# Optimization experiments

Hardware: AMD Instinct MI355X
Metric: run time of the kernel (lower is better)

The kernel has to match this reference:

```python
import jax, jax.numpy as jnp
import numpy as np

B, L, EMB, U, V = 128, 64, 512, 1024, 50257
BN_EPS = 0.001


def setup_inputs() -> dict:
    key = jax.random.key(0)
    ks = jax.random.split(key, 20)
    s = 0.02
    return {
        "x": jax.random.randint(ks[0], (B, 1), 0, V, dtype=jnp.int64),
        "features": jax.random.normal(ks[1], (B, L, EMB), jnp.float32),
        "hidden": jax.random.normal(ks[2], (1, B, U), jnp.float32),
        "emb_table": jax.random.normal(ks[3], (V, EMB), jnp.float32) * s,
        "Uattn_w": jax.random.normal(ks[4], (U, EMB), jnp.float32) * s,
        "Uattn_b": jnp.zeros((U,), jnp.float32),
        "Wattn_w": jax.random.normal(ks[5], (U, U), jnp.float32) * s,
        "Wattn_b": jnp.zeros((U,), jnp.float32),
        "Vattn_w": jax.random.normal(ks[6], (1, U), jnp.float32) * s,
        "Vattn_b": jnp.zeros((1,), jnp.float32),
        "W_ih": jax.random.normal(ks[7], (3 * U, U), jnp.float32) * s,
        "W_hh": jax.random.normal(ks[8], (3 * U, U), jnp.float32) * s,
        "b_ih": jnp.zeros((3 * U,), jnp.float32),
        "b_hh": jnp.zeros((3 * U,), jnp.float32),
        "fc_w": jax.random.normal(ks[9], (U, U), jnp.float32) * s,
        "fc_b": jnp.zeros((U,), jnp.float32),
        "bn_gamma": jnp.ones((U,), jnp.float32),
        "bn_beta": jnp.zeros((U,), jnp.float32),
        "bn_mean": jnp.zeros((U,), jnp.float32),
        "bn_var": jnp.ones((U,), jnp.float32),
        "fc2_w": jax.random.normal(ks[10], (V, U), jnp.float32) * s,
        "fc2_b": jnp.zeros((V,), jnp.float32),
    }


def reference(x, features, hidden, emb_table, Uattn_w, Uattn_b, Wattn_w, Wattn_b,
              Vattn_w, Vattn_b, W_ih, W_hh, b_ih, b_hh, fc_w, fc_b,
              bn_gamma, bn_beta, bn_mean, bn_var, fc2_w, fc2_b):
    h = hidden[0]  # [B, U]
    # Bahdanau attention
    Uf = jnp.einsum('ble,ue->blu', features, Uattn_w) + Uattn_b        # [B,L,U]
    Wh = h @ Wattn_w.T + Wattn_b                                        # [B,U]
    score = jnp.tanh(Uf + Wh[:, None, :]) @ Vattn_w.T + Vattn_b        # [B,L,1]
    attn = jax.nn.softmax(score, axis=1)                                # [B,L,1]
    ctx = jnp.sum(attn * features, axis=1)                              # [B,EMB]
    # embed token and concat -> GRU input (seq len 1)
    e = emb_table[x[:, 0]]                                              # [B,EMB]
    gin = jnp.concatenate([ctx, e], axis=-1)                            # [B,U]
    # single-step GRU (PyTorch gate convention)
    gi = gin @ W_ih.T + b_ih                                            # [B,3U]
    gh = h @ W_hh.T + b_hh                                              # [B,3U]
    i_r, i_z, i_n = jnp.split(gi, 3, axis=-1)
    h_r, h_z, h_n = jnp.split(gh, 3, axis=-1)
    r = jax.nn.sigmoid(i_r + h_r)
    z = jax.nn.sigmoid(i_z + h_z)
    n = jnp.tanh(i_n + r * h_n)
    h_new = (1.0 - z) * n + z * h                                       # [B,U]
    # head: fc -> (dropout: identity in eval) -> BN (eval) -> fc2
    y = h_new @ fc_w.T + fc_b
    y = (y - bn_mean) * jax.lax.rsqrt(bn_var + BN_EPS) * bn_gamma + bn_beta
    logits = y @ fc2_w.T + fc2_b                                        # [B,V]
    return logits, h_new[None, :, :], attn
```

## Files before the change

### kernel.cpp

```cpp
#include <hip/hip_runtime.h>

typedef short bf8 __attribute__((ext_vector_type(8)));
typedef float f32x4 __attribute__((ext_vector_type(4)));

__device__ inline short f2bfs(float f) {
    unsigned u = __builtin_bit_cast(unsigned, f);
    u += 0x7FFFu + ((u >> 16) & 1u);
    return (short)(u >> 16);
}

__device__ inline unsigned pk2(float x, float y) {
    return (unsigned)(unsigned short)f2bfs(x) |
           ((unsigned)(unsigned short)f2bfs(y) << 16);
}

__device__ inline float bf2f(short s) {
    unsigned u = ((unsigned)(unsigned short)s) << 16;
    return __builtin_bit_cast(float, u);
}

__device__ inline bf8 cvt_frag(f32x4 lo, f32x4 hi) {
    union { bf8 v; unsigned u[4]; } r;
    r.u[0] = pk2(lo[0], lo[1]);
    r.u[1] = pk2(lo[2], lo[3]);
    r.u[2] = pk2(hi[0], hi[1]);
    r.u[3] = pk2(hi[2], hi[3]);
    return r.v;
}

__device__ inline float fast_tanh(float x) {
    x = fminf(fmaxf(x, -15.f), 15.f);
    float e = __expf(2.f * x);
    return (e - 1.f) / (e + 1.f);
}

__device__ inline void gl_lds16(const void* g, void* l) {
    __builtin_amdgcn_global_load_lds(
        (const __attribute__((address_space(1))) unsigned int*)g,
        (__attribute__((address_space(3))) unsigned int*)l,
        16, 0, 0);
}

#define BAR() asm volatile("s_barrier" ::: "memory")

template<int N> __device__ __forceinline__ void waitvm() {
    if constexpr (N == 8)      asm volatile("s_waitcnt vmcnt(8)"  ::: "memory");
    else if constexpr (N == 6) asm volatile("s_waitcnt vmcnt(6)"  ::: "memory");
    else if constexpr (N == 4) asm volatile("s_waitcnt vmcnt(4)"  ::: "memory");
    else if constexpr (N == 3) asm volatile("s_waitcnt vmcnt(3)"  ::: "memory");
    else                       asm volatile("s_waitcnt vmcnt(0)"  ::: "memory");
}

#define MFMA16 __builtin_amdgcn_mfma_f32_16x16x32_bf16

template<int EPI, int BM_, bool OBF>
__device__ __forceinline__ void gemm_body(
    char* smem,
    const short* __restrict__ A, const float* __restrict__ W,
    const float* __restrict__ bias, void* __restrict__ Cv,
    int N, int K, int lda, int n0, int m0,
    const float* __restrict__ q0, const float* __restrict__ q1,
    const float* __restrict__ q2, const float* __restrict__ q3,
    float* __restrict__ score)
{
    constexpr int FM  = BM_ / 32;
    constexpr int ATS = BM_ * 64;
    constexpr int LPT = (BM_ == 128) ? 4 : 3;

    const int lane = threadIdx.x & 63;
    const int wave = threadIdx.x >> 6;
    const int wm0  = (wave >> 1) * (BM_ / 2);
    const int wn0  = (wave & 1) * 32;
    const int lr   = lane & 15;
    const int g    = lane >> 4;

    f32x4 acc[FM][2] = {};

    auto stage = [&](int buf, int k0) {
        char* sA = smem + buf * ATS;
        char* sW = smem + 3 * ATS + buf * 8192;
        #pragma unroll
        for (int cc = 0; cc < BM_ / 64; ++cc) {
            int c  = wave * (BM_ / 64) + cc;
            int r  = c * 16 + (lane >> 2);
            int ss = (lane & 3) ^ ((r >> 1) & 3);
            gl_lds16(&A[(size_t)(m0 + r) * lda + k0 + ss * 8], sA + c * 1024);
        }
        #pragma unroll
        for (int cc = 0; cc < 2; ++cc) {
            int c  = wave * 2 + cc;
            int r  = c * 8 + (lane >> 3);
            int ss = (lane & 7) ^ (r & 7);
            int rg = n0 + r; rg = rg < N ? rg : N - 1;
            gl_lds16(&W[(size_t)rg * K + k0 + ss * 4], sW + c * 1024);
        }
    };

    auto compute = [&](int buf) {
        char* sA = smem + buf * ATS;
        char* sW = smem + 3 * ATS + buf * 8192;
        bf8 av[FM], bv[2];
        #pragma unroll
        for (int i = 0; i < FM; ++i) {
            int ra = wm0 + i * 16 + lr;
            int sl = g ^ ((ra >> 1) & 3);
            av[i] = *reinterpret_cast<const bf8*>(sA + ra * 64 + sl * 16);
        }
        #pragma unroll
        for (int j = 0; j < 2; ++j) {
            int rb = wn0 + j * 16 + lr;
            int l0 = (2 * g)     ^ (rb & 7);
            int l1 = (2 * g + 1) ^ (rb & 7);
            f32x4 lo = *reinterpret_cast<const f32x4*>(sW + rb * 128 + l0 * 16);
            f32x4 hi = *reinterpret_cast<const f32x4*>(sW + rb * 128 + l1 * 16);
            bv[j] = cvt_frag(lo, hi);
        }
        #pragma unroll
        for (int i = 0; i < FM; ++i)
            #pragma unroll
            for (int j = 0; j < 2; ++j)
                acc[i][j] = MFMA16(av[i], bv[j], acc[i][j], 0, 0, 0);
    };

    const int nt = K >> 5;
    stage(0, 0); stage(1, 32);
    int bs = 2, bc = 0;
    for (int t = 0; t < nt - 2; ++t) {
        stage(bs, (t + 2) << 5);
        bs = (bs == 2) ? 0 : bs + 1;
        waitvm<2 * LPT>(); BAR();
        compute(bc);
        bc = (bc == 2) ? 0 : bc + 1;
        BAR();
    }
    waitvm<1 * LPT>(); BAR(); compute(bc); bc = (bc == 2) ? 0 : bc + 1; BAR();
    waitvm<0>();       BAR(); compute(bc);

    if constexpr (EPI == 2) {
        #pragma unroll
        for (int i = 0; i < FM; ++i) {
            #pragma unroll
            for (int r = 0; r < 4; ++r) {
                int m = m0 + wm0 + i * 16 + g * 4 + r;
                int bidx = m >> 6;
                float s = 0.f;
                #pragma unroll
                for (int j = 0; j < 2; ++j) {
                    int n = n0 + wn0 + j * 16 + lr;
                    s += fast_tanh(acc[i][j][r] + bias[n] + q0[(size_t)bidx * N + n]) * q1[n];
                }
                #pragma unroll
                for (int off = 1; off < 16; off <<= 1)
                    s += __shfl_xor(s, off);
                if (lr == 0) atomicAdd(&score[m], s);
            }
        }
    } else {
        #pragma unroll
        for (int j = 0; j < 2; ++j) {
            int n = n0 + wn0 + j * 16 + lr;
            if (n >= N) continue;
            float bn_ = bias[n];
            float sc = 1.f, sh = 0.f;
            if constexpr (EPI == 1) {
                sc = q0[n] * rsqrtf(q3[n] + 1e-3f);
                sh = q1[n] - q2[n] * sc;
            }
            #pragma unroll
            for (int i = 0; i < FM; ++i) {
                #pragma unroll
                for (int r = 0; r < 4; ++r) {
                    int m = m0 + wm0 + i * 16 + g * 4 + r;
                    float v = acc[i][j][r] + bn_;
                    if constexpr (EPI == 1) v = v * sc + sh;
                    if constexpr (OBF) ((short*)Cv)[(size_t)m * N + n] = f2bfs(v);
                    else               ((float*)Cv)[(size_t)m * N + n] = v;
                }
            }
        }
    }
}

template<int EPI, int BM_, bool OBF>
__global__ __launch_bounds__(256) void gemm_k(
    const short* __restrict__ A, const float* __restrict__ W,
    const float* __restrict__ bias, void* __restrict__ Cv,
    int N, int K, int lda,
    const float* __restrict__ q0, const float* __restrict__ q1,
    const float* __restrict__ q2, const float* __restrict__ q3,
    float* __restrict__ score)
{
    __shared__ __align__(1024) char smem[3 * BM_ * 64 + 3 * 8192];
    gemm_body<EPI, BM_, OBF>(smem, A, W, bias, Cv, N, K, lda,
                             blockIdx.x * 64, blockIdx.y * BM_,
                             q0, q1, q2, q3, score);
}

__global__ __launch_bounds__(256) void gemm_dual(
    const short* __restrict__ A0, const float* __restrict__ W0,
    const float* __restrict__ b0, float* __restrict__ C0,
    const short* __restrict__ A1, const float* __restrict__ W1,
    const float* __restrict__ b1, float* __restrict__ C1,
    int N, int K, int lda)
{
    __shared__ __align__(1024) char smem[3 * 64 * 64 + 3 * 8192];
    if (blockIdx.z == 0)
        gemm_body<0, 64, false>(smem, A0, W0, b0, C0, N, K, lda,
                                blockIdx.x * 64, blockIdx.y * 64,
                                nullptr, nullptr, nullptr, nullptr, nullptr);
    else
        gemm_body<0, 64, false>(smem, A1, W1, b1, C1, N, K, lda,
                                blockIdx.x * 64, blockIdx.y * 64,
                                nullptr, nullptr, nullptr, nullptr, nullptr);
}

__global__ __launch_bounds__(256) void prep_all(
    const float* __restrict__ feat, short* __restrict__ feat_bf,
    const float* __restrict__ h, short* __restrict__ h_bf,
    float* __restrict__ score, const float* __restrict__ vb)
{
    int t = blockIdx.x * 256 + threadIdx.x;
    {
        float4 v0 = *reinterpret_cast<const float4*>(feat + (size_t)t * 8);
        float4 v1 = *reinterpret_cast<const float4*>(feat + (size_t)t * 8 + 4);
        uint4 q = make_uint4(pk2(v0.x, v0.y), pk2(v0.z, v0.w),
                             pk2(v1.x, v1.y), pk2(v1.z, v1.w));
        *reinterpret_cast<uint4*>(feat_bf + (size_t)t * 8) = q;
    }
    if (t < 16384) {
        float4 v0 = *reinterpret_cast<const float4*>(h + (size_t)t * 8);
        float4 v1 = *reinterpret_cast<const float4*>(h + (size_t)t * 8 + 4);
        uint4 q = make_uint4(pk2(v0.x, v0.y), pk2(v0.z, v0.w),
                             pk2(v1.x, v1.y), pk2(v1.z, v1.w));
        *reinterpret_cast<uint4*>(h_bf + (size_t)t * 8) = q;
    }
    if (t < 1024) {
        float v = vb[0];
        float4 vv = make_float4(v, v, v, v);
        *reinterpret_cast<float4*>(score + t * 8)     = vv;
        *reinterpret_cast<float4*>(score + t * 8 + 4) = vv;
    }
}

__global__ __launch_bounds__(256) void softmax_ctx(
    const float* __restrict__ score, const short* __restrict__ feat_bf,
    const int* __restrict__ x, const float* __restrict__ emb,
    float* __restrict__ attn_out, short* __restrict__ gin_bf)
{
    int b = blockIdx.x;
    int t = threadIdx.x;
    __shared__ float sa[64];
    if (t < 64) {
        float v = score[b * 64 + t];
        float m = v;
        #pragma unroll
        for (int off = 32; off; off >>= 1) m = fmaxf(m, __shfl_xor(m, off));
        float e = __expf(v - m);
        float s = e;
        #pragma unroll
        for (int off = 32; off; off >>= 1) s += __shfl_xor(s, off);
        float a = e / s;
        attn_out[b * 64 + t] = a;
        sa[t] = a;
    }
    __syncthreads();
    {
        int e0 = t * 2;
        float c0 = 0.f, c1 = 0.f;
        #pragma unroll 4
        for (int l = 0; l < 64; ++l) {
            float a = sa[l];
            unsigned v = *reinterpret_cast<const unsigned*>(
                &feat_bf[((size_t)b * 64 + l) * 512 + e0]);
            c0 += a * bf2f((short)(v & 0xffff));
            c1 += a * bf2f((short)(v >> 16));
        }
        *reinterpret_cast<unsigned*>(&gin_bf[(size_t)b * 1024 + e0]) = pk2(c0, c1);
    }
    {
        int xi = x[b];
        int e0 = t * 2;
        float2 ev = *reinterpret_cast<const float2*>(&emb[(size_t)xi * 512 + e0]);
        *reinterpret_cast<unsigned*>(&gin_bf[(size_t)b * 1024 + 512 + e0]) = pk2(ev.x, ev.y);
    }
}

__global__ __launch_bounds__(256) void gru_kernel(
    const float* __restrict__ gi, const float* __restrict__ gh,
    const float* __restrict__ h, float* __restrict__ hnew,
    short* __restrict__ hnew_bf)
{
    int idx = blockIdx.x * 256 + threadIdx.x;
    int b = idx >> 10, u = idx & 1023;
    const float* gib = gi + (size_t)b * 3072;
    const float* ghb = gh + (size_t)b * 3072;
    float ir = gib[u], iz = gib[1024 + u], in_ = gib[2048 + u];
    float hr = ghb[u], hz = ghb[1024 + u], hn = ghb[2048 + u];
    float r = 1.f / (1.f + __expf(-(ir + hr)));
    float z = 1.f / (1.f + __expf(-(iz + hz)));
    float n = fast_tanh(in_ + r * hn);
    float val = (1.f - z) * n + z * h[idx];
    hnew[idx] = val;
    hnew_bf[idx] = f2bfs(val);
}

extern "C" void kernel_launch(void* const* d_in, const int* in_sizes, int n_in,
                              void* d_out, int out_size, void* d_ws, size_t ws_size,
                              hipStream_t stream)
{
    const int*   x        = (const int*)  d_in[0];
    const float* features = (const float*)d_in[1];
    const float* hidden   = (const float*)d_in[2];
    const float* emb      = (const float*)d_in[3];
    const float* Uattn_w  = (const float*)d_in[4];
    const float* Uattn_b  = (const float*)d_in[5];
    const float* Wattn_w  = (const float*)d_in[6];
    const float* Wattn_b  = (const float*)d_in[7];
    const float* Vattn_w  = (const float*)d_in[8];
    const float* Vattn_b  = (const float*)d_in[9];
    const float* W_ih     = (const float*)d_in[10];
    const float* W_hh     = (const float*)d_in[11];
    const float* b_ih     = (const float*)d_in[12];
    const float* b_hh     = (const float*)d_in[13];
    const float* fc_w     = (const float*)d_in[14];
    const float* fc_b     = (const float*)d_in[15];
    const float* bn_gamma = (const float*)d_in[16];
    const float* bn_beta  = (const float*)d_in[17];
    const float* bn_mean  = (const float*)d_in[18];
    const float* bn_var   = (const float*)d_in[19];
    const float* fc2_w    = (const float*)d_in[20];
    const float* fc2_b    = (const float*)d_in[21];

    float* out    = (float*)d_out;
    float* logits = out;
    float* hnew   = out + 6432896;
    float* attn   = out + 6432896 + 131072;

    float* ws        = (float*)d_ws;
    float* Wh        = ws;
    float* scoreb    = ws + 131072;
    float* gi        = ws + 139264;
    float* gh        = ws + 532480;
    short* hidden_bf = (short*)(ws + 925696);
    short* gin_bf    = (short*)(ws + 991232);
    short* hnew_bf   = (short*)(ws + 1056768);
    short* y_bf      = (short*)(ws + 1122304);
    short* feat_bf   = (short*)(ws + 1187840);

    prep_all<<<2048, 256, 0, stream>>>(features, feat_bf, hidden, hidden_bf,
                                       scoreb, Vattn_b);

    gemm_k<0, 64, false><<<dim3(16, 2), 256, 0, stream>>>(
        hidden_bf, Wattn_w, Wattn_b, Wh, 1024, 1024, 1024,
        nullptr, nullptr, nullptr, nullptr, nullptr);

    gemm_k<2, 128, false><<<dim3(16, 64), 256, 0, stream>>>(
        feat_bf, Uattn_w, Uattn_b, nullptr, 1024, 512, 512,
        Wh, Vattn_w, nullptr, nullptr, scoreb);

    softmax_ctx<<<128, 256, 0, stream>>>(scoreb, feat_bf, x, emb, attn, gin_bf);

    gemm_dual<<<dim3(48, 2, 2), 256, 0, stream>>>(
        gin_bf, W_ih, b_ih, gi,
        hidden_bf, W_hh, b_hh, gh, 3072, 1024, 1024);

    gru_kernel<<<512, 256, 0, stream>>>(gi, gh, hidden, hnew, hnew_bf);

    gemm_k<1, 64, true><<<dim3(16, 2), 256, 0, stream>>>(
        hnew_bf, fc_w, fc_b, y_bf, 1024, 1024, 1024,
        bn_gamma, bn_beta, bn_mean, bn_var, nullptr);

    gemm_k<0, 128, false><<<dim3(786, 1), 256, 0, stream>>>(
        y_bf, fc2_w, fc2_b, logits, 50257, 1024, 1024,
        nullptr, nullptr, nullptr, nullptr, nullptr);
}
```

Measured before the change: 150.6 us.

## Add dedicated fc2 GEMM kernel with 64x64 tiles and 3-stage deeper K pipeline

Replaces the generic gemm_k launch for the vocab projection with a specialized kernel using 64x64 output tiles, K-step 64, and a 3-buffer async global-to-LDS pipeline. The grid is split over M into two blocks per N tile, which doubles the block count to raise occupancy and latency hiding. In exchange, each fc2 weight tile is now read by two blocks instead of one, which doubles weight traffic unless L2 serves the second read, and the fp32-to-bf16 weight conversion is repeated per block.

```diff
diff --git a/kernel.cpp b/kernel.cpp
--- a/kernel.cpp
+++ b/kernel.cpp
@@ -44,7 +44,8 @@
 #define BAR() asm volatile("s_barrier" ::: "memory")
 
 template<int N> __device__ __forceinline__ void waitvm() {
-    if constexpr (N == 8)      asm volatile("s_waitcnt vmcnt(8)"  ::: "memory");
+    if constexpr (N == 12)     asm volatile("s_waitcnt vmcnt(12)" ::: "memory");
+    else if constexpr (N == 8) asm volatile("s_waitcnt vmcnt(8)"  ::: "memory");
     else if constexpr (N == 6) asm volatile("s_waitcnt vmcnt(6)"  ::: "memory");
     else if constexpr (N == 4) asm volatile("s_waitcnt vmcnt(4)"  ::: "memory");
     else if constexpr (N == 3) asm volatile("s_waitcnt vmcnt(3)"  ::: "memory");
@@ -212,6 +213,101 @@
         gemm_body<0, 64, false>(smem, A1, W1, b1, C1, N, K, lda,
                                 blockIdx.x * 64, blockIdx.y * 64,
                                 nullptr, nullptr, nullptr, nullptr, nullptr);
+}
+
+__global__ __launch_bounds__(256) void gemm_fc2(
+    const short* __restrict__ A, const float* __restrict__ W,
+    const float* __restrict__ bias, float* __restrict__ C, int N, int K)
+{
+    __shared__ __align__(1024) char smem[3 * 8192 + 3 * 16384];
+    const int lane = threadIdx.x & 63;
+    const int wave = threadIdx.x >> 6;
+    const int wm0  = (wave >> 1) * 32;
+    const int wn0  = (wave & 1) * 32;
+    const int lr   = lane & 15;
+    const int g    = lane >> 4;
+    const int n0   = blockIdx.x * 64;
+    const int m0   = blockIdx.y * 64;
+
+    f32x4 acc[2][2] = {};
+
+    auto stage = [&](int buf, int k0) {
+        char* sA = smem + buf * 8192;
+        char* sW = smem + 3 * 8192 + buf * 16384;
+        #pragma unroll
+        for (int cc = 0; cc < 2; ++cc) {
+            int c  = wave * 2 + cc;
+            int r  = c * 8 + (lane >> 3);
+            int ss = (lane & 7) ^ (r & 7);
+            gl_lds16(&A[(size_t)(m0 + r) * K + k0 + ss * 8], sA + c * 1024);
+        }
+        #pragma unroll
+        for (int cc = 0; cc < 4; ++cc) {
+            int c  = wave * 4 + cc;
+            int r  = c * 4 + (lane >> 4);
+            int ss = (lane & 15) ^ (r & 15);
+            int rg = n0 + r; rg = rg < N ? rg : N - 1;
+            gl_lds16(&W[(size_t)rg * K + k0 + ss * 4], sW + c * 1024);
+        }
+    };
+
+    auto compute = [&](int buf) {
+        char* sA = smem + buf * 8192;
+        char* sW = smem + 3 * 8192 + buf * 16384;
+        #pragma unroll
+        for (int ks = 0; ks < 2; ++ks) {
+            bf8 av[2], bv[2];
+            #pragma unroll
+            for (int i = 0; i < 2; ++i) {
+                int ra = wm0 + i * 16 + lr;
+                int sl = (ks * 4 + g) ^ (ra & 7);
+                av[i] = *reinterpret_cast<const bf8*>(sA + ra * 128 + sl * 16);
+            }
+            #pragma unroll
+            for (int j = 0; j < 2; ++j) {
+                int rb = wn0 + j * 16 + lr;
+                int s0 = (ks * 8 + g * 2)     ^ (rb & 15);
+                int s1 = (ks * 8 + g * 2 + 1) ^ (rb & 15);
+                f32x4 lo = *reinterpret_cast<const f32x4*>(sW + rb * 256 + s0 * 16);
+                f32x4 hi = *reinterpret_cast<const f32x4*>(sW + rb * 256 + s1 * 16);
+                bv[j] = cvt_frag(lo, hi);
+            }
+            #pragma unroll
+            for (int i = 0; i < 2; ++i)
+                #pragma unroll
+                for (int j = 0; j < 2; ++j)
+                    acc[i][j] = MFMA16(av[i], bv[j], acc[i][j], 0, 0, 0);
+        }
+    };
+
+    const int nt = K >> 6;
+    stage(0, 0); stage(1, 64);
+    int bs = 2, bc = 0;
+    for (int t = 0; t < nt - 2; ++t) {
+        stage(bs, (t + 2) << 6);
+        bs = (bs == 2) ? 0 : bs + 1;
+        waitvm<12>(); BAR();
+        compute(bc);
+        bc = (bc == 2) ? 0 : bc + 1;
+        BAR();
+    }
+    waitvm<6>(); BAR(); compute(bc); bc = (bc == 2) ? 0 : bc + 1; BAR();
+    waitvm<0>(); BAR(); compute(bc);
+
+    #pragma unroll
+    for (int j = 0; j < 2; ++j) {
+        int n = n0 + wn0 + j * 16 + lr;
+        if (n >= N) continue;
+        float bn_ = bias[n];
+        #pragma unroll
+        for (int i = 0; i < 2; ++i) {
+            #pragma unroll
+            for (int r = 0; r < 4; ++r) {
+                int m = m0 + wm0 + i * 16 + g * 4 + r;
+                C[(size_t)m * N + n] = acc[i][j][r] + bn_;
+            }
+        }
+    }
 }
 
 __global__ __launch_bounds__(256) void prep_all(
@@ -370,7 +466,5 @@
         hnew_bf, fc_w, fc_b, y_bf, 1024, 1024, 1024,
         bn_gamma, bn_beta, bn_mean, bn_var, nullptr);
 
-    gemm_k<0, 128, false><<<dim3(786, 1), 256, 0, stream>>>(
-        y_bf, fc2_w, fc2_b, logits, 50257, 1024, 1024,
-        nullptr, nullptr, nullptr, nullptr, nullptr);
-}
+    gemm_fc2<<<dim3(786, 2), 256, 0, stream>>>(y_bf, fc2_w, fc2_b, logits, 50257, 1024);
+}
```

Result: slower. 158.4 us (+5.2%).
